# Kernel tuning notes

Hardware: AMD Instinct MI355X
Metric: run time of the kernel (lower is better)

The kernel has to match this reference:

```python
import jax, jax.numpy as jnp
import numpy as np

TEMPERATURE_F = 0.5  # temperature_f from __init__


def setup_inputs() -> dict:
    key = jax.random.key(0)
    k1, k2 = jax.random.split(key)
    B, D = 4096, 512
    h_i = jax.random.normal(k1, (B, D), dtype=jnp.float32)
    h_j = jax.random.normal(k2, (B, D), dtype=jnp.float32)
    return {"h_i": h_i, "h_j": h_j}


def reference(h_i, h_j) -> jnp.ndarray:
    # NT-Xent loss (forward_private). N = 2*batch_size.
    B = h_i.shape[0]
    N = 2 * B
    h = jnp.concatenate([h_i, h_j], axis=0)          # [N, D]
    sim = (h @ h.T) / TEMPERATURE_F                   # [N, N]

    # Positive pairs: sim[i, i+B] and sim[i+B, i]
    sim_i_j = jnp.diagonal(sim, offset=B)             # [B]
    sim_j_i = jnp.diagonal(sim, offset=-B)            # [B]
    pos = jnp.concatenate([sim_i_j, sim_j_i], axis=0)  # [N]

    # Original builds logits = [pos | negatives] where negatives are the row of
    # sim with the diagonal and the positive entry removed, and labels are 0.
    # Cross-entropy per row = -pos_i + logsumexp(pos_i, negatives_i)
    #                       = -pos_i + logsumexp over row i of sim excluding the
    #                         diagonal (the positive entry equals pos_i, so the
    #                         set of logsumexp'd values is identical).
    neg_inf = jnp.finfo(sim.dtype).min
    diag = jnp.eye(N, dtype=bool)
    sim_masked = jnp.where(diag, neg_inf, sim)        # exclude self-similarity
    lse = jax.nn.logsumexp(sim_masked, axis=1)        # [N]

    loss = jnp.sum(lse - pos) / N                     # CE sum reduction, / N
    return loss
```

## Files before the change

kernel.cpp:

```cpp
#include <hip/hip_runtime.h>
#include <hip/hip_bf16.h>
#include <float.h>

#define BN_ 4096
#define DD  512
#define NN  8192
#define SCALE 2.0f

typedef unsigned short u16;
typedef __attribute__((ext_vector_type(8))) short short8;
typedef __attribute__((ext_vector_type(4))) float floatx4;

struct alignas(8) U16x4 { u16 x, y, z, w; };

__device__ __forceinline__ u16 f2bf(float f) {
    union { float f; unsigned u; } c; c.f = f;
    unsigned u = c.u;
    unsigned r = (u + 0x7fffu + ((u >> 16) & 1u)) >> 16;
    return (u16)r;
}

__device__ __forceinline__ void async_copy16(const u16* g, u16* l) {
    __builtin_amdgcn_global_load_lds(
        (const __attribute__((address_space(1))) void*)g,
        (__attribute__((address_space(3))) void*)l, 16, 0, 0);
}

__global__ __launch_bounds__(256) void convert_pos_kernel(const float* __restrict__ hi,
                                                          const float* __restrict__ hj,
                                                          u16* __restrict__ H,
                                                          float* __restrict__ Pos,
                                                          float* __restrict__ out) {
    __shared__ float red[4];
    int t = blockIdx.x * 256 + threadIdx.x;
    int e = t * 4;
    const int BD = BN_ * DD;
    float4 a = *(const float4*)(hi + e);
    float4 b = *(const float4*)(hj + e);
    U16x4 oa, ob;
    oa.x = f2bf(a.x); oa.y = f2bf(a.y); oa.z = f2bf(a.z); oa.w = f2bf(a.w);
    ob.x = f2bf(b.x); ob.y = f2bf(b.y); ob.z = f2bf(b.z); ob.w = f2bf(b.w);
    *(U16x4*)(H + e) = oa;
    *(U16x4*)(H + BD + e) = ob;
    float dot = a.x * b.x + a.y * b.y + a.z * b.z + a.w * b.w;
#pragma unroll
    for (int msk = 1; msk < 64; msk <<= 1) dot += __shfl_xor(dot, msk);
    int lane = threadIdx.x & 63, wid = threadIdx.x >> 6;
    if (lane == 0) red[wid] = dot;
    __syncthreads();
    if (threadIdx.x == 0) {
        Pos[blockIdx.x] = red[0] + red[1] + red[2] + red[3];
        if (blockIdx.x == 0) *out = 0.0f;
    }
}

__global__ __launch_bounds__(256, 3) void gram_kernel(const u16* __restrict__ H,
                                                      float* __restrict__ Mpart,
                                                      float* __restrict__ Spart) {
    __shared__ u16 As[128 * 64];
    __shared__ u16 Bs[128 * 64];
    __shared__ float Rm[2][128], Rs[2][128];
    __shared__ float Cm[2][128], Cs[2][128];

    const int tid  = threadIdx.x;
    const int lane = tid & 63;
    const int wid  = tid >> 6;
    const int quad = lane >> 4;
    const int ln15 = lane & 15;
    const int wr = wid >> 1, wc = wid & 1;

    int t = blockIdx.x;
    int bi = (int)((sqrtf(8.0f * (float)t + 1.0f) - 1.0f) * 0.5f);
    while ((bi + 1) * (bi + 2) / 2 <= t) bi++;
    while (bi * (bi + 1) / 2 > t) bi--;
    const int bj = t - bi * (bi + 1) / 2;
    const bool diag = (bi == bj);
    const int biBase = bi * 128, bjBase = bj * 128;

    const u16* srcA[4];
    int ldsOff[4];
#pragma unroll
    for (int j = 0; j < 4; j++) {
        int c   = j * 256 + tid;
        int row = c >> 3;
        int kc  = (c & 7) ^ (row & 7);
        srcA[j]   = H + (size_t)(biBase + row) * DD + kc * 8;
        ldsOff[j] = c * 8;
    }
    const ptrdiff_t dB = (ptrdiff_t)(bjBase - biBase) * DD;

    floatx4 acc[4][4];
#pragma unroll
    for (int i = 0; i < 4; i++)
#pragma unroll
        for (int j = 0; j < 4; j++) acc[i][j] = (floatx4)0.0f;

    for (int k0 = 0; k0 < DD; k0 += 64) {
#pragma unroll
        for (int j = 0; j < 4; j++) async_copy16(srcA[j] + k0,      &As[ldsOff[j]]);
#pragma unroll
        for (int j = 0; j < 4; j++) async_copy16(srcA[j] + dB + k0, &Bs[ldsOff[j]]);
        __syncthreads();

#pragma unroll
        for (int kk = 0; kk < 2; kk++) {
            int ck = kk * 4 + quad;
            short8 a[4], b[4];
#pragma unroll
            for (int tm = 0; tm < 4; tm++) {
                int r = wr * 64 + tm * 16 + ln15;
                a[tm] = *(const short8*)&As[(r * 8 + (ck ^ (r & 7))) * 8];
            }
#pragma unroll
            for (int tn = 0; tn < 4; tn++) {
                int r = wc * 64 + tn * 16 + ln15;
                b[tn] = *(const short8*)&Bs[(r * 8 + (ck ^ (r & 7))) * 8];
            }
#pragma unroll
            for (int tm = 0; tm < 4; tm++)
#pragma unroll
                for (int tn = 0; tn < 4; tn++)
                    acc[tm][tn] = __builtin_amdgcn_mfma_f32_16x16x32_bf16(
                        a[tm], b[tn], acc[tm][tn], 0, 0, 0);
        }
        __syncthreads();
    }

#pragma unroll
    for (int tm = 0; tm < 4; tm++)
#pragma unroll
        for (int tn = 0; tn < 4; tn++)
#pragma unroll
            for (int r = 0; r < 4; r++) {
                float v = SCALE * acc[tm][tn][r];
                if (diag) {
                    int lrow = wr * 64 + tm * 16 + quad * 4 + r;
                    int lcol = wc * 64 + tn * 16 + ln15;
                    if (lrow == lcol) v = -FLT_MAX;
                }
                acc[tm][tn][r] = v;
            }

#pragma unroll
    for (int tm = 0; tm < 4; tm++) {
#pragma unroll
        for (int r = 0; r < 4; r++) {
            float vmax = -FLT_MAX;
#pragma unroll
            for (int tn = 0; tn < 4; tn++) vmax = fmaxf(vmax, acc[tm][tn][r]);
#pragma unroll
            for (int msk = 1; msk < 16; msk <<= 1)
                vmax = fmaxf(vmax, __shfl_xor(vmax, msk));
            float s = 0.0f;
#pragma unroll
            for (int tn = 0; tn < 4; tn++) s += __expf(acc[tm][tn][r] - vmax);
#pragma unroll
            for (int msk = 1; msk < 16; msk <<= 1) s += __shfl_xor(s, msk);
            if (ln15 == 0) {
                int x = wr * 64 + tm * 16 + quad * 4 + r;
                Rm[wc][x] = vmax; Rs[wc][x] = s;
            }
        }
    }

    if (!diag) {
#pragma unroll
        for (int tn = 0; tn < 4; tn++) {
            float cm = -FLT_MAX;
#pragma unroll
            for (int tm = 0; tm < 4; tm++)
#pragma unroll
                for (int r = 0; r < 4; r++) cm = fmaxf(cm, acc[tm][tn][r]);
            cm = fmaxf(cm, __shfl_xor(cm, 16));
            cm = fmaxf(cm, __shfl_xor(cm, 32));
            float s = 0.0f;
#pragma unroll
            for (int tm = 0; tm < 4; tm++)
#pragma unroll
                for (int r = 0; r < 4; r++) s += __expf(acc[tm][tn][r] - cm);
            s += __shfl_xor(s, 16);
            s += __shfl_xor(s, 32);
            if (quad == 0) {
                int y = wc * 64 + tn * 16 + ln15;
                Cm[wr][y] = cm; Cs[wr][y] = s;
            }
        }
    }
    __syncthreads();

    if (tid < 128) {
        float m0 = Rm[0][tid], m1 = Rm[1][tid];
        float s0 = Rs[0][tid], s1 = Rs[1][tid];
        float m = fmaxf(m0, m1);
        float s = s0 * __expf(m0 - m) + s1 * __expf(m1 - m);
        Mpart[(size_t)bj * NN + biBase + tid] = m;
        Spart[(size_t)bj * NN + biBase + tid] = s;
    } else if (!diag) {
        int y = tid - 128;
        float m0 = Cm[0][y], m1 = Cm[1][y];
        float s0 = Cs[0][y], s1 = Cs[1][y];
        float m = fmaxf(m0, m1);
        float s = s0 * __expf(m0 - m) + s1 * __expf(m1 - m);
        Mpart[(size_t)bi * NN + bjBase + y] = m;
        Spart[(size_t)bi * NN + bjBase + y] = s;
    }
}

__global__ __launch_bounds__(256) void lse_kernel(const float* __restrict__ Mpart,
                                                  const float* __restrict__ Spart,
                                                  const float* __restrict__ Pos,
                                                  float* __restrict__ out) {
    __shared__ float red[256];
    int tid = threadIdx.x;
    int r = blockIdx.x * 256 + tid;
    float m = -FLT_MAX, s = 0.0f;
#pragma unroll 8
    for (int c = 0; c < 64; c++) {
        float mc = Mpart[(size_t)c * NN + r];
        float sc = Spart[(size_t)c * NN + r];
        float mn = fmaxf(m, mc);
        s = s * __expf(m - mn) + sc * __expf(mc - mn);
        m = mn;
    }
    float v = m + logf(s);
    if (tid < 64) v += -4.0f * Pos[blockIdx.x * 64 + tid];
    red[tid] = v;
    __syncthreads();
    for (int st = 128; st > 0; st >>= 1) {
        if (tid < st) red[tid] += red[tid + st];
        __syncthreads();
    }
    if (tid == 0) atomicAdd(out, red[0] * (1.0f / (float)NN));
}

extern "C" void kernel_launch(void* const* d_in, const int* in_sizes, int n_in,
                              void* d_out, int out_size, void* d_ws, size_t ws_size,
                              hipStream_t stream) {
    const float* hi = (const float*)d_in[0];
    const float* hj = (const float*)d_in[1];
    float* out = (float*)d_out;

    u16*   H     = (u16*)d_ws;
    float* Mpart = (float*)((char*)d_ws + (size_t)8 * 1024 * 1024);
    float* Spart = (float*)((char*)d_ws + (size_t)10 * 1024 * 1024);
    float* Pos   = (float*)((char*)d_ws + (size_t)12 * 1024 * 1024);

    convert_pos_kernel<<<2048, 256, 0, stream>>>(hi, hj, H, Pos, out);

    gram_kernel<<<2080, 256, 0, stream>>>(H, Mpart, Spart);

    lse_kernel<<<32, 256, 0, stream>>>(Mpart, Spart, Pos, out);
}
```

Baseline: 129.5 us.

## Double-buffer B tile in LDS and load A fragments directly from global

The gram kernel stops staging the A tile in shared memory. Each wave now reads its A fragments straight from global memory into registers, and the freed LDS is used to double-buffer the B tile so the next k-slice's async copy overlaps the current MFMAs, with one barrier per iteration. The goal is to hide global-load latency and halve the barriers. In exchange, each A element is read from global/L2 by both column waves (duplicate traffic), there are more VGPRs for the a[2][4] fragments, and the direct global loads are not coalesced in a tile-friendly way.

```diff
diff --git a/kernel.cpp b/kernel.cpp
--- a/kernel.cpp
+++ b/kernel.cpp
@@ -57,8 +57,7 @@
 __global__ __launch_bounds__(256, 3) void gram_kernel(const u16* __restrict__ H,
                                                       float* __restrict__ Mpart,
                                                       float* __restrict__ Spart) {
-    __shared__ u16 As[128 * 64];
-    __shared__ u16 Bs[128 * 64];
+    __shared__ u16 Bs[2][128 * 64];
     __shared__ float Rm[2][128], Rs[2][128];
     __shared__ float Cm[2][128], Cs[2][128];
 
@@ -77,17 +76,21 @@
     const bool diag = (bi == bj);
     const int biBase = bi * 128, bjBase = bj * 128;
 
-    const u16* srcA[4];
-    int ldsOff[4];
+    const u16* srcB[4];
+    int dstB[4];
 #pragma unroll
     for (int j = 0; j < 4; j++) {
         int c   = j * 256 + tid;
         int row = c >> 3;
         int kc  = (c & 7) ^ (row & 7);
-        srcA[j]   = H + (size_t)(biBase + row) * DD + kc * 8;
-        ldsOff[j] = c * 8;
-    }
-    const ptrdiff_t dB = (ptrdiff_t)(bjBase - biBase) * DD;
+        srcB[j] = H + (size_t)(bjBase + row) * DD + kc * 8;
+        dstB[j] = c * 8;
+    }
+
+    const u16* aRow[4];
+#pragma unroll
+    for (int tm = 0; tm < 4; tm++)
+        aRow[tm] = H + (size_t)(biBase + wr * 64 + tm * 16 + ln15) * DD + quad * 8;
 
     floatx4 acc[4][4];
 #pragma unroll
@@ -95,35 +98,41 @@
 #pragma unroll
         for (int j = 0; j < 4; j++) acc[i][j] = (floatx4)0.0f;
 
-    for (int k0 = 0; k0 < DD; k0 += 64) {
-#pragma unroll
-        for (int j = 0; j < 4; j++) async_copy16(srcA[j] + k0,      &As[ldsOff[j]]);
-#pragma unroll
-        for (int j = 0; j < 4; j++) async_copy16(srcA[j] + dB + k0, &Bs[ldsOff[j]]);
+#pragma unroll
+    for (int j = 0; j < 4; j++) async_copy16(srcB[j], &Bs[0][dstB[j]]);
+
+    for (int i = 0; i < 8; i++) {
         __syncthreads();
-
+        const int k0 = i * 64;
+        short8 a[2][4];
+#pragma unroll
+        for (int kk = 0; kk < 2; kk++)
+#pragma unroll
+            for (int tm = 0; tm < 4; tm++)
+                a[kk][tm] = *(const short8*)(aRow[tm] + k0 + kk * 32);
+        if (i < 7) {
+            const int nxt = (i + 1) & 1;
+#pragma unroll
+            for (int j = 0; j < 4; j++)
+                async_copy16(srcB[j] + k0 + 64, &Bs[nxt][dstB[j]]);
+        }
+        const u16* bs = Bs[i & 1];
 #pragma unroll
         for (int kk = 0; kk < 2; kk++) {
             int ck = kk * 4 + quad;
-            short8 a[4], b[4];
-#pragma unroll
-            for (int tm = 0; tm < 4; tm++) {
-                int r = wr * 64 + tm * 16 + ln15;
-                a[tm] = *(const short8*)&As[(r * 8 + (ck ^ (r & 7))) * 8];
-            }
+            short8 b[4];
 #pragma unroll
             for (int tn = 0; tn < 4; tn++) {
                 int r = wc * 64 + tn * 16 + ln15;
-                b[tn] = *(const short8*)&Bs[(r * 8 + (ck ^ (r & 7))) * 8];
+                b[tn] = *(const short8*)&bs[(r * 8 + (ck ^ (r & 7))) * 8];
             }
 #pragma unroll
             for (int tm = 0; tm < 4; tm++)
 #pragma unroll
                 for (int tn = 0; tn < 4; tn++)
                     acc[tm][tn] = __builtin_amdgcn_mfma_f32_16x16x32_bf16(
-                        a[tm], b[tn], acc[tm][tn], 0, 0, 0);
-        }
-        __syncthreads();
+                        a[kk][tm], b[tn], acc[tm][tn], 0, 0, 0);
+        }
     }
 
 #pragma unroll
```

New measurement: 166.2 us. 28.3% more time.

## Fuse convert, gram, and LSE stages into one persistent cooperative kernel

Applied to the files above, without the earlier changes.

Replaces three kernel launches with one cooperative persistent kernel. It grid-strides over the bf16 conversion and positive-dot work, then over the 2080 triangular gram tiles, then does the final logsumexp reduction, with grid.sync between the phases. The aim is to remove launch gaps and the tail effects between stages. In exchange it adds a cooperative-launch and occupancy query on every call, two grid-wide barriers, a fixed persistent grid that may balance tiles less evenly, and a serial Pos sum in block 0.

```diff
diff --git a/kernel.cpp b/kernel.cpp
--- a/kernel.cpp
+++ b/kernel.cpp
@@ -1,6 +1,9 @@
 #include <hip/hip_runtime.h>
+#include <hip/hip_cooperative_groups.h>
 #include <hip/hip_bf16.h>
 #include <float.h>
+
+namespace cg = cooperative_groups;
 
 #define BN_ 4096
 #define DD  512
@@ -26,211 +29,221 @@
         (__attribute__((address_space(3))) void*)l, 16, 0, 0);
 }
 
-__global__ __launch_bounds__(256) void convert_pos_kernel(const float* __restrict__ hi,
-                                                          const float* __restrict__ hj,
-                                                          u16* __restrict__ H,
-                                                          float* __restrict__ Pos,
-                                                          float* __restrict__ out) {
-    __shared__ float red[4];
-    int t = blockIdx.x * 256 + threadIdx.x;
-    int e = t * 4;
-    const int BD = BN_ * DD;
-    float4 a = *(const float4*)(hi + e);
-    float4 b = *(const float4*)(hj + e);
-    U16x4 oa, ob;
-    oa.x = f2bf(a.x); oa.y = f2bf(a.y); oa.z = f2bf(a.z); oa.w = f2bf(a.w);
-    ob.x = f2bf(b.x); ob.y = f2bf(b.y); ob.z = f2bf(b.z); ob.w = f2bf(b.w);
-    *(U16x4*)(H + e) = oa;
-    *(U16x4*)(H + BD + e) = ob;
-    float dot = a.x * b.x + a.y * b.y + a.z * b.z + a.w * b.w;
-#pragma unroll
-    for (int msk = 1; msk < 64; msk <<= 1) dot += __shfl_xor(dot, msk);
-    int lane = threadIdx.x & 63, wid = threadIdx.x >> 6;
-    if (lane == 0) red[wid] = dot;
-    __syncthreads();
-    if (threadIdx.x == 0) {
-        Pos[blockIdx.x] = red[0] + red[1] + red[2] + red[3];
-        if (blockIdx.x == 0) *out = 0.0f;
-    }
-}
-
-__global__ __launch_bounds__(256, 3) void gram_kernel(const u16* __restrict__ H,
-                                                      float* __restrict__ Mpart,
-                                                      float* __restrict__ Spart) {
+__global__ __launch_bounds__(256, 3) void fused_kernel(const float* __restrict__ hi,
+                                                       const float* __restrict__ hj,
+                                                       u16* __restrict__ H,
+                                                       float* __restrict__ Mpart,
+                                                       float* __restrict__ Spart,
+                                                       float* __restrict__ Pos,
+                                                       float* __restrict__ out) {
     __shared__ u16 As[128 * 64];
     __shared__ u16 Bs[128 * 64];
     __shared__ float Rm[2][128], Rs[2][128];
     __shared__ float Cm[2][128], Cs[2][128];
 
+    cg::grid_group grid = cg::this_grid();
     const int tid  = threadIdx.x;
+    const int bid  = blockIdx.x;
+    const int nB   = gridDim.x;
     const int lane = tid & 63;
     const int wid  = tid >> 6;
     const int quad = lane >> 4;
     const int ln15 = lane & 15;
     const int wr = wid >> 1, wc = wid & 1;
-
-    int t = blockIdx.x;
-    int bi = (int)((sqrtf(8.0f * (float)t + 1.0f) - 1.0f) * 0.5f);
-    while ((bi + 1) * (bi + 2) / 2 <= t) bi++;
-    while (bi * (bi + 1) / 2 > t) bi--;
-    const int bj = t - bi * (bi + 1) / 2;
-    const bool diag = (bi == bj);
-    const int biBase = bi * 128, bjBase = bj * 128;
-
-    const u16* srcA[4];
-    int ldsOff[4];
-#pragma unroll
-    for (int j = 0; j < 4; j++) {
-        int c   = j * 256 + tid;
-        int row = c >> 3;
-        int kc  = (c & 7) ^ (row & 7);
-        srcA[j]   = H + (size_t)(biBase + row) * DD + kc * 8;
-        ldsOff[j] = c * 8;
-    }
-    const ptrdiff_t dB = (ptrdiff_t)(bjBase - biBase) * DD;
-
-    floatx4 acc[4][4];
-#pragma unroll
-    for (int i = 0; i < 4; i++)
-#pragma unroll
-        for (int j = 0; j < 4; j++) acc[i][j] = (floatx4)0.0f;
-
-    for (int k0 = 0; k0 < DD; k0 += 64) {
-#pragma unroll
-        for (int j = 0; j < 4; j++) async_copy16(srcA[j] + k0,      &As[ldsOff[j]]);
-#pragma unroll
-        for (int j = 0; j < 4; j++) async_copy16(srcA[j] + dB + k0, &Bs[ldsOff[j]]);
-        __syncthreads();
-
-#pragma unroll
-        for (int kk = 0; kk < 2; kk++) {
-            int ck = kk * 4 + quad;
-            short8 a[4], b[4];
-#pragma unroll
-            for (int tm = 0; tm < 4; tm++) {
-                int r = wr * 64 + tm * 16 + ln15;
-                a[tm] = *(const short8*)&As[(r * 8 + (ck ^ (r & 7))) * 8];
+    const int BD = BN_ * DD;
+
+    float dotAcc = 0.0f;
+    for (int chunk = bid; chunk < 2048; chunk += nB) {
+        int e = (chunk * 256 + tid) * 4;
+        float4 a = *(const float4*)(hi + e);
+        float4 b = *(const float4*)(hj + e);
+        U16x4 oa, ob;
+        oa.x = f2bf(a.x); oa.y = f2bf(a.y); oa.z = f2bf(a.z); oa.w = f2bf(a.w);
+        ob.x = f2bf(b.x); ob.y = f2bf(b.y); ob.z = f2bf(b.z); ob.w = f2bf(b.w);
+        *(U16x4*)(H + e) = oa;
+        *(U16x4*)(H + BD + e) = ob;
+        dotAcc += a.x * b.x + a.y * b.y + a.z * b.z + a.w * b.w;
+    }
+#pragma unroll
+    for (int msk = 1; msk < 64; msk <<= 1) dotAcc += __shfl_xor(dotAcc, msk);
+    {
+        float* red = &Rm[0][0];
+        if (lane == 0) red[wid] = dotAcc;
+        __syncthreads();
+        if (tid == 0) {
+            Pos[bid] = red[0] + red[1] + red[2] + red[3];
+            if (bid == 0) *out = 0.0f;
+        }
+    }
+    __threadfence();
+    grid.sync();
+
+    for (int t = bid; t < 2080; t += nB) {
+        int bi = (int)((sqrtf(8.0f * (float)t + 1.0f) - 1.0f) * 0.5f);
+        while ((bi + 1) * (bi + 2) / 2 <= t) bi++;
+        while (bi * (bi + 1) / 2 > t) bi--;
+        const int bj = t - bi * (bi + 1) / 2;
+        const bool diag = (bi == bj);
+        const int biBase = bi * 128, bjBase = bj * 128;
+
+        const u16* srcA[4];
+        int ldsOff[4];
+#pragma unroll
+        for (int j = 0; j < 4; j++) {
+            int c   = j * 256 + tid;
+            int row = c >> 3;
+            int kc  = (c & 7) ^ (row & 7);
+            srcA[j]   = H + (size_t)(biBase + row) * DD + kc * 8;
+            ldsOff[j] = c * 8;
+        }
+        const ptrdiff_t dB = (ptrdiff_t)(bjBase - biBase) * DD;
+
+        floatx4 acc[4][4];
+#pragma unroll
+        for (int i = 0; i < 4; i++)
+#pragma unroll
+            for (int j = 0; j < 4; j++) acc[i][j] = (floatx4)0.0f;
+
+        for (int k0 = 0; k0 < DD; k0 += 64) {
+#pragma unroll
+            for (int j = 0; j < 4; j++) async_copy16(srcA[j] + k0,      &As[ldsOff[j]]);
+#pragma unroll
+            for (int j = 0; j < 4; j++) async_copy16(srcA[j] + dB + k0, &Bs[ldsOff[j]]);
+            __syncthreads();
+
+#pragma unroll
+            for (int kk = 0; kk < 2; kk++) {
+                int ck = kk * 4 + quad;
+                short8 a[4], b[4];
+#pragma unroll
+                for (int tm = 0; tm < 4; tm++) {
+                    int r = wr * 64 + tm * 16 + ln15;
+                    a[tm] = *(const short8*)&As[(r * 8 + (ck ^ (r & 7))) * 8];
+                }
+#pragma unroll
+                for (int tn = 0; tn < 4; tn++) {
+                    int r = wc * 64 + tn * 16 + ln15;
+                    b[tn] = *(const short8*)&Bs[(r * 8 + (ck ^ (r & 7))) * 8];
+                }
+#pragma unroll
+                for (int tm = 0; tm < 4; tm++)
+#pragma unroll
+                    for (int tn = 0; tn < 4; tn++)
+                        acc[tm][tn] = __builtin_amdgcn_mfma_f32_16x16x32_bf16(
+                            a[tm], b[tn], acc[tm][tn], 0, 0, 0);
             }
+            __syncthreads();
+        }
+
+#pragma unroll
+        for (int tm = 0; tm < 4; tm++)
+#pragma unroll
+            for (int tn = 0; tn < 4; tn++)
+#pragma unroll
+                for (int r = 0; r < 4; r++) {
+                    float v = SCALE * acc[tm][tn][r];
+                    if (diag) {
+                        int lrow = wr * 64 + tm * 16 + quad * 4 + r;
+                        int lcol = wc * 64 + tn * 16 + ln15;
+                        if (lrow == lcol) v = -FLT_MAX;
+                    }
+                    acc[tm][tn][r] = v;
+                }
+
+#pragma unroll
+        for (int tm = 0; tm < 4; tm++) {
+#pragma unroll
+            for (int r = 0; r < 4; r++) {
+                float vmax = -FLT_MAX;
+#pragma unroll
+                for (int tn = 0; tn < 4; tn++) vmax = fmaxf(vmax, acc[tm][tn][r]);
+#pragma unroll
+                for (int msk = 1; msk < 16; msk <<= 1)
+                    vmax = fmaxf(vmax, __shfl_xor(vmax, msk));
+                float s = 0.0f;
+#pragma unroll
+                for (int tn = 0; tn < 4; tn++) s += __expf(acc[tm][tn][r] - vmax);
+#pragma unroll
+                for (int msk = 1; msk < 16; msk <<= 1) s += __shfl_xor(s, msk);
+                if (ln15 == 0) {
+                    int x = wr * 64 + tm * 16 + quad * 4 + r;
+                    Rm[wc][x] = vmax; Rs[wc][x] = s;
+                }
+            }
+        }
+
+        if (!diag) {
 #pragma unroll
             for (int tn = 0; tn < 4; tn++) {
-                int r = wc * 64 + tn * 16 + ln15;
-                b[tn] = *(const short8*)&Bs[(r * 8 + (ck ^ (r & 7))) * 8];
+                float cm = -FLT_MAX;
+#pragma unroll
+                for (int tm = 0; tm < 4; tm++)
+#pragma unroll
+                    for (int r = 0; r < 4; r++) cm = fmaxf(cm, acc[tm][tn][r]);
+                cm = fmaxf(cm, __shfl_xor(cm, 16));
+                cm = fmaxf(cm, __shfl_xor(cm, 32));
+                float s = 0.0f;
+#pragma unroll
+                for (int tm = 0; tm < 4; tm++)
+#pragma unroll
+                    for (int r = 0; r < 4; r++) s += __expf(acc[tm][tn][r] - cm);
+                s += __shfl_xor(s, 16);
+                s += __shfl_xor(s, 32);
+                if (quad == 0) {
+                    int y = wc * 64 + tn * 16 + ln15;
+                    Cm[wr][y] = cm; Cs[wr][y] = s;
+                }
             }
-#pragma unroll
-            for (int tm = 0; tm < 4; tm++)
-#pragma unroll
-                for (int tn = 0; tn < 4; tn++)
-                    acc[tm][tn] = __builtin_amdgcn_mfma_f32_16x16x32_bf16(
-                        a[tm], b[tn], acc[tm][tn], 0, 0, 0);
-        }
-        __syncthreads();
-    }
-
-#pragma unroll
-    for (int tm = 0; tm < 4; tm++)
-#pragma unroll
-        for (int tn = 0; tn < 4; tn++)
-#pragma unroll
-            for (int r = 0; r < 4; r++) {
-                float v = SCALE * acc[tm][tn][r];
-                if (diag) {
-                    int lrow = wr * 64 + tm * 16 + quad * 4 + r;
-                    int lcol = wc * 64 + tn * 16 + ln15;
-                    if (lrow == lcol) v = -FLT_MAX;
-                }
-                acc[tm][tn][r] = v;
-            }
-
-#pragma unroll
-    for (int tm = 0; tm < 4; tm++) {
-#pragma unroll
-        for (int r = 0; r < 4; r++) {
-            float vmax = -FLT_MAX;
-#pragma unroll
-            for (int tn = 0; tn < 4; tn++) vmax = fmaxf(vmax, acc[tm][tn][r]);
-#pragma unroll
-            for (int msk = 1; msk < 16; msk <<= 1)
-                vmax = fmaxf(vmax, __shfl_xor(vmax, msk));
-            float s = 0.0f;
-#pragma unroll
-            for (int tn = 0; tn < 4; tn++) s += __expf(acc[tm][tn][r] - vmax);
-#pragma unroll
-            for (int msk = 1; msk < 16; msk <<= 1) s += __shfl_xor(s, msk);
-            if (ln15 == 0) {
-                int x = wr * 64 + tm * 16 + quad * 4 + r;
-                Rm[wc][x] = vmax; Rs[wc][x] = s;
-            }
-        }
-    }
-
-    if (!diag) {
-#pragma unroll
-        for (int tn = 0; tn < 4; tn++) {
-            float cm = -FLT_MAX;
-#pragma unroll
-            for (int tm = 0; tm < 4; tm++)
-#pragma unroll
-                for (int r = 0; r < 4; r++) cm = fmaxf(cm, acc[tm][tn][r]);
-            cm = fmaxf(cm, __shfl_xor(cm, 16));
-            cm = fmaxf(cm, __shfl_xor(cm, 32));
-            float s = 0.0f;
-#pragma unroll
-            for (int tm = 0; tm < 4; tm++)
-#pragma unroll
-                for (int r = 0; r < 4; r++) s += __expf(acc[tm][tn][r] - cm);
-            s += __shfl_xor(s, 16);
-            s += __shfl_xor(s, 32);
-            if (quad == 0) {
-                int y = wc * 64 + tn * 16 + ln15;
-                Cm[wr][y] = cm; Cs[wr][y] = s;
-            }
-        }
-    }
-    __syncthreads();
-
-    if (tid < 128) {
-        float m0 = Rm[0][tid], m1 = Rm[1][tid];
-        float s0 = Rs[0][tid], s1 = Rs[1][tid];
-        float m = fmaxf(m0, m1);
-        float s = s0 * __expf(m0 - m) + s1 * __expf(m1 - m);
-        Mpart[(size_t)bj * NN + biBase + tid] = m;
-        Spart[(size_t)bj * NN + biBase + tid] = s;
-    } else if (!diag) {
-        int y = tid - 128;
-        float m0 = Cm[0][y], m1 = Cm[1][y];
-        float s0 = Cs[0][y], s1 = Cs[1][y];
-        float m = fmaxf(m0, m1);
-        float s = s0 * __expf(m0 - m) + s1 * __expf(m1 - m);
-        Mpart[(size_t)bi * NN + bjBase + y] = m;
-        Spart[(size_t)bi * NN + bjBase + y] = s;
-    }
-}
-
-__global__ __launch_bounds__(256) void lse_kernel(const float* __restrict__ Mpart,
-                                                  const float* __restrict__ Spart,
-                                                  const float* __restrict__ Pos,
-                                                  float* __restrict__ out) {
-    __shared__ float red[256];
-    int tid = threadIdx.x;
-    int r = blockIdx.x * 256 + tid;
-    float m = -FLT_MAX, s = 0.0f;
+        }
+        __syncthreads();
+
+        if (tid < 128) {
+            float m0 = Rm[0][tid], m1 = Rm[1][tid];
+            float s0 = Rs[0][tid], s1 = Rs[1][tid];
+            float m = fmaxf(m0, m1);
+            float s = s0 * __expf(m0 - m) + s1 * __expf(m1 - m);
+            Mpart[(size_t)bj * NN + biBase + tid] = m;
+            Spart[(size_t)bj * NN + biBase + tid] = s;
+        } else if (!diag) {
+            int y = tid - 128;
+            float m0 = Cm[0][y], m1 = Cm[1][y];
+            float s0 = Cs[0][y], s1 = Cs[1][y];
+            float m = fmaxf(m0, m1);
+            float s = s0 * __expf(m0 - m) + s1 * __expf(m1 - m);
+            Mpart[(size_t)bi * NN + bjBase + y] = m;
+            Spart[(size_t)bi * NN + bjBase + y] = s;
+        }
+        __syncthreads();
+    }
+    __threadfence();
+    grid.sync();
+
+    if (bid < 32) {
+        int r = bid * 256 + tid;
+        float m = -FLT_MAX, s = 0.0f;
 #pragma unroll 8
-    for (int c = 0; c < 64; c++) {
-        float mc = Mpart[(size_t)c * NN + r];
-        float sc = Spart[(size_t)c * NN + r];
-        float mn = fmaxf(m, mc);
-        s = s * __expf(m - mn) + sc * __expf(mc - mn);
-        m = mn;
-    }
-    float v = m + logf(s);
-    if (tid < 64) v += -4.0f * Pos[blockIdx.x * 64 + tid];
-    red[tid] = v;
-    __syncthreads();
-    for (int st = 128; st > 0; st >>= 1) {
-        if (tid < st) red[tid] += red[tid + st];
-        __syncthreads();
-    }
-    if (tid == 0) atomicAdd(out, red[0] * (1.0f / (float)NN));
+        for (int c = 0; c < 64; c++) {
+            float mc = Mpart[(size_t)c * NN + r];
+            float sc = Spart[(size_t)c * NN + r];
+            float mn = fmaxf(m, mc);
+            s = s * __expf(m - mn) + sc * __expf(mc - mn);
+            m = mn;
+        }
+        float v = m + logf(s);
+        if (bid == 0) {
+            float p = 0.0f;
+            for (int i = tid; i < nB; i += 256) p += Pos[i];
+            v += -4.0f * p;
+        }
+        float* red = &Rm[0][0];
+        red[tid] = v;
+        __syncthreads();
+        for (int st = 128; st > 0; st >>= 1) {
+            if (tid < st) red[tid] += red[tid + st];
+            __syncthreads();
+        }
+        if (tid == 0) atomicAdd(out, red[0] * (1.0f / (float)NN));
+    }
 }
 
 extern "C" void kernel_launch(void* const* d_in, const int* in_sizes, int n_in,
@@ -245,9 +258,13 @@
     float* Spart = (float*)((char*)d_ws + (size_t)10 * 1024 * 1024);
     float* Pos   = (float*)((char*)d_ws + (size_t)12 * 1024 * 1024);
 
-    convert_pos_kernel<<<2048, 256, 0, stream>>>(hi, hj, H, Pos, out);
-
-    gram_kernel<<<2080, 256, 0, stream>>>(H, Mpart, Spart);
-
-    lse_kernel<<<32, 256, 0, stream>>>(Mpart, Spart, Pos, out);
-}
+    int nb = 0;
+    hipOccupancyMaxActiveBlocksPerMultiprocessor(&nb, fused_kernel, 256, 0);
+    int grid = nb * 256;
+    if (grid > 768) grid = 768;
+    if (grid < 256) grid = 256;
+
+    void* args[7] = {(void*)&hi, (void*)&hj, (void*)&H, (void*)&Mpart,
+                     (void*)&Spart, (void*)&Pos, (void*)&out};
+    hipLaunchCooperativeKernel(fused_kernel, dim3(grid), dim3(256), args, 0, stream);
+}
```

New measurement: 308.4 us. 138% more time.

## Fuse final logsumexp reduction into gram kernel via last-blocks completion counter

Applied to the files above, without the earlier changes.

Removes the separate lse_kernel launch. Each gram tile block increments a global counter after writing its partials, and the last 32 blocks to finish spin until every tile is done, then perform the per-row logsumexp merge and the atomic loss accumulation. This saves one kernel launch and its dependency gap. In exchange it relies on a spin-wait on an atomic counter with memory fences. The Pos sum is regrouped by row segment so that the blocks handling segment 0 add all positive terms.

```diff
diff --git a/kernel.cpp b/kernel.cpp
--- a/kernel.cpp
+++ b/kernel.cpp
@@ -6,6 +6,8 @@
 #define DD  512
 #define NN  8192
 #define SCALE 2.0f
+#define NTILES 2080
+#define NLSE   32
 
 typedef unsigned short u16;
 typedef __attribute__((ext_vector_type(8))) short short8;
@@ -30,6 +32,7 @@
                                                           const float* __restrict__ hj,
                                                           u16* __restrict__ H,
                                                           float* __restrict__ Pos,
+                                                          unsigned* __restrict__ done,
                                                           float* __restrict__ out) {
     __shared__ float red[4];
     int t = blockIdx.x * 256 + threadIdx.x;
@@ -50,17 +53,21 @@
     __syncthreads();
     if (threadIdx.x == 0) {
         Pos[blockIdx.x] = red[0] + red[1] + red[2] + red[3];
-        if (blockIdx.x == 0) *out = 0.0f;
+        if (blockIdx.x == 0) { *out = 0.0f; *done = 0u; }
     }
 }
 
 __global__ __launch_bounds__(256, 3) void gram_kernel(const u16* __restrict__ H,
                                                       float* __restrict__ Mpart,
-                                                      float* __restrict__ Spart) {
+                                                      float* __restrict__ Spart,
+                                                      const float* __restrict__ Pos,
+                                                      unsigned* __restrict__ done,
+                                                      float* __restrict__ out) {
     __shared__ u16 As[128 * 64];
     __shared__ u16 Bs[128 * 64];
     __shared__ float Rm[2][128], Rs[2][128];
     __shared__ float Cm[2][128], Cs[2][128];
+    __shared__ unsigned ordShared;
 
     const int tid  = threadIdx.x;
     const int lane = tid & 63;
@@ -204,33 +211,51 @@
         Mpart[(size_t)bi * NN + bjBase + y] = m;
         Spart[(size_t)bi * NN + bjBase + y] = s;
     }
-}
-
-__global__ __launch_bounds__(256) void lse_kernel(const float* __restrict__ Mpart,
-                                                  const float* __restrict__ Spart,
-                                                  const float* __restrict__ Pos,
-                                                  float* __restrict__ out) {
-    __shared__ float red[256];
-    int tid = threadIdx.x;
-    int r = blockIdx.x * 256 + tid;
-    float m = -FLT_MAX, s = 0.0f;
+
+    __threadfence();
+    __syncthreads();
+    if (tid == 0) ordShared = atomicAdd(done, 1u);
+    __syncthreads();
+    const unsigned ord = ordShared;
+    if (ord < NTILES - NLSE) return;
+    const int seg = (int)(ord - (NTILES - NLSE));
+
+    if (tid == 0) {
+        while (__hip_atomic_load(done, __ATOMIC_ACQUIRE,
+                                 __HIP_MEMORY_SCOPE_AGENT) < NTILES) {
+            __builtin_amdgcn_s_sleep(8);
+        }
+    }
+    __syncthreads();
+    __threadfence();
+
+    {
+        int r = seg * 256 + tid;
+        float m = -FLT_MAX, s = 0.0f;
 #pragma unroll 8
-    for (int c = 0; c < 64; c++) {
-        float mc = Mpart[(size_t)c * NN + r];
-        float sc = Spart[(size_t)c * NN + r];
-        float mn = fmaxf(m, mc);
-        s = s * __expf(m - mn) + sc * __expf(mc - mn);
-        m = mn;
-    }
-    float v = m + logf(s);
-    if (tid < 64) v += -4.0f * Pos[blockIdx.x * 64 + tid];
-    red[tid] = v;
-    __syncthreads();
-    for (int st = 128; st > 0; st >>= 1) {
-        if (tid < st) red[tid] += red[tid + st];
+        for (int c = 0; c < 64; c++) {
+            float mc = Mpart[(size_t)c * NN + r];
+            float sc = Spart[(size_t)c * NN + r];
+            float mn = fmaxf(m, mc);
+            s = s * __expf(m - mn) + sc * __expf(mc - mn);
+            m = mn;
+        }
+        float v = m + logf(s);
+        if (seg == 0) {
+            float p = 0.0f;
+#pragma unroll
+            for (int i = 0; i < 8; i++) p += Pos[tid * 8 + i];
+            v += -4.0f * p;
+        }
+        float* red = &Rm[0][0];
+        red[tid] = v;
         __syncthreads();
-    }
-    if (tid == 0) atomicAdd(out, red[0] * (1.0f / (float)NN));
+        for (int st = 128; st > 0; st >>= 1) {
+            if (tid < st) red[tid] += red[tid + st];
+            __syncthreads();
+        }
+        if (tid == 0) atomicAdd(out, red[0] * (1.0f / (float)NN));
+    }
 }
 
 extern "C" void kernel_launch(void* const* d_in, const int* in_sizes, int n_in,
@@ -240,14 +265,13 @@
     const float* hj = (const float*)d_in[1];
     float* out = (float*)d_out;
 
-    u16*   H     = (u16*)d_ws;
-    float* Mpart = (float*)((char*)d_ws + (size_t)8 * 1024 * 1024);
-    float* Spart = (float*)((char*)d_ws + (size_t)10 * 1024 * 1024);
-    float* Pos   = (float*)((char*)d_ws + (size_t)12 * 1024 * 1024);
-
-    convert_pos_kernel<<<2048, 256, 0, stream>>>(hi, hj, H, Pos, out);
-
-    gram_kernel<<<2080, 256, 0, stream>>>(H, Mpart, Spart);
-
-    lse_kernel<<<32, 256, 0, stream>>>(Mpart, Spart, Pos, out);
-}
+    u16*      H     = (u16*)d_ws;
+    float*    Mpart = (float*)((char*)d_ws + (size_t)8 * 1024 * 1024);
+    float*    Spart = (float*)((char*)d_ws + (size_t)10 * 1024 * 1024);
+    float*    Pos   = (float*)((char*)d_ws + (size_t)12 * 1024 * 1024);
+    unsigned* done  = (unsigned*)((char*)d_ws + (size_t)12 * 1024 * 1024 + 16384);
+
+    convert_pos_kernel<<<2048, 256, 0, stream>>>(hi, hj, H, Pos, done, out);
+
+    gram_kernel<<<NTILES, 256, 0, stream>>>(H, Mpart, Spart, Pos, done, out);
+}
```

New measurement: 285.6 us. 121% more time.
